# Performance work log

Measured on AMD Instinct MI355X. Metric: run time of the kernel, lower is better.

## Reference

```python
import jax, jax.numpy as jnp
import numpy as np
from jax import lax

FH, FW, STRIDE = 100, 160, 16
IMG_H, IMG_W = FH * STRIDE, FW * STRIDE
A = 9
PRE_NMS, POST_NMS = 6000, 300  # prediction-path caps (training=0)
IOU_THR = 0.7
NEG = jnp.float32(-1e9)


def _make_anchor_map():
    # classic 3 scales x 3 aspect ratios, stride-16 grid, (y1,x1,y2,x2)
    scales = np.array([128.0, 256.0, 512.0], np.float32)
    ratios = np.array([0.5, 1.0, 2.0], np.float32)
    hs = (scales[:, None] * np.sqrt(ratios)[None, :]).reshape(-1)  # [9]
    ws = (scales[:, None] / np.sqrt(ratios)[None, :]).reshape(-1)
    cy = ((np.arange(FH, dtype=np.float32) + 0.5) * STRIDE)[:, None, None]
    cx = ((np.arange(FW, dtype=np.float32) + 0.5) * STRIDE)[None, :, None]
    y1 = np.broadcast_to(cy - 0.5 * hs, (FH, FW, A))
    x1 = np.broadcast_to(cx - 0.5 * ws, (FH, FW, A))
    y2 = np.broadcast_to(cy + 0.5 * hs, (FH, FW, A))
    x2 = np.broadcast_to(cx + 0.5 * ws, (FH, FW, A))
    am = np.stack([y1, x1, y2, x2], axis=-1)  # [FH,FW,9,4]
    return jnp.asarray(am.reshape(1, FH, FW, A * 4))


def setup_inputs() -> dict:
    key = jax.random.key(0)
    ks = jax.random.split(key, 6)
    return {
        "input_image": jax.random.uniform(ks[0], (1, IMG_H, IMG_W, 3), jnp.float32),
        "feature_map": jax.random.normal(ks[1], (1, FH, FW, 512), jnp.float32),
        "anchor_map": _make_anchor_map(),
        "anchor_valid_map": jnp.ones((1, FH, FW, A), jnp.float32),
        "W1": 0.01 * jax.random.normal(ks[2], (3, 3, 512, 512), jnp.float32),
        "b1": jnp.zeros((512,), jnp.float32),
        "Wc": 0.01 * jax.random.normal(ks[3], (1, 1, 512, A), jnp.float32),
        "bc": jnp.zeros((A,), jnp.float32),
        "Wr": 0.01 * jax.random.normal(ks[4], (1, 1, 512, 4 * A), jnp.float32),
        "br": jnp.zeros((4 * A,), jnp.float32),
        "training": 0,
    }


def _conv(x, w, b):
    return lax.conv_general_dilated(
        x, w, (1, 1), "SAME", dimension_numbers=("NHWC", "HWIO", "NHWC")
    ) + b


def _iou_one_vs_all(box, boxes):
    yy1 = jnp.maximum(box[0], boxes[:, 0])
    xx1 = jnp.maximum(box[1], boxes[:, 1])
    yy2 = jnp.minimum(box[2], boxes[:, 2])
    xx2 = jnp.minimum(box[3], boxes[:, 3])
    inter = jnp.maximum(yy2 - yy1, 0.0) * jnp.maximum(xx2 - xx1, 0.0)
    a1 = jnp.maximum(box[2] - box[0], 0.0) * jnp.maximum(box[3] - box[1], 0.0)
    a2 = jnp.maximum(boxes[:, 2] - boxes[:, 0], 0.0) * jnp.maximum(boxes[:, 3] - boxes[:, 1], 0.0)
    return inter / (a1 + a2 - inter + 1e-8)


def _nms(boxes, scores, max_out, iou_thr):
    # greedy NMS with fixed iteration count (padded with zero boxes)
    def step(s, _):
        i = jnp.argmax(s)
        best = s[i]
        box = boxes[i]
        valid = best > NEG * 0.5
        ious = _iou_one_vs_all(box, boxes)
        s = jnp.where(ious > iou_thr, NEG, s)
        s = s.at[i].set(NEG)
        out = jnp.where(valid, box, jnp.zeros_like(box))
        return s, out

    _, sel = lax.scan(step, scores, None, length=max_out)
    return sel  # [max_out, 4]


def reference(input_image, feature_map, anchor_map, anchor_valid_map,
              W1, b1, Wc, bc, Wr, br, training):
    pre_nms = 12000 if training else PRE_NMS
    post_nms = 2000 if training else POST_NMS
    # RPN head convs
    y = jax.nn.relu(_conv(feature_map, W1, b1))
    scores_map = jax.nn.sigmoid(_conv(y, Wc, bc))          # [1,FH,FW,9]
    reg_map = _conv(y, Wr, br)                              # [1,FH,FW,36]
    # flatten (extract_valid)
    anchors = anchor_map.reshape(-1, 4)                     # [N,4] (y1,x1,y2,x2)
    obj = scores_map.reshape(-1)                            # [N]
    deltas = reg_map.reshape(-1, 4)                         # [N,4] (ty,tx,th,tw)
    # delta -> bbox decode (means=0, stds=1)
    ah = anchors[:, 2] - anchors[:, 0]
    aw = anchors[:, 3] - anchors[:, 1]
    acy = anchors[:, 0] + 0.5 * ah
    acx = anchors[:, 1] + 0.5 * aw
    cy = acy + deltas[:, 0] * ah
    cx = acx + deltas[:, 1] * aw
    h = ah * jnp.exp(deltas[:, 2])
    w = aw * jnp.exp(deltas[:, 3])
    props = jnp.stack([cy - 0.5 * h, cx - 0.5 * w, cy + 0.5 * h, cx + 0.5 * w], axis=1)
    # sort desc by score, keep top pre_nms
    sc, idx = lax.top_k(obj, pre_nms)
    props = props[idx]
    # clip to image
    img_h = jnp.float32(input_image.shape[1])
    img_w = jnp.float32(input_image.shape[2])
    tl = jnp.maximum(props[:, 0:2], 0.0)
    y2 = jnp.minimum(props[:, 2], img_h)[:, None]
    x2 = jnp.minimum(props[:, 3], img_w)[:, None]
    props = jnp.concatenate([tl, y2, x2], axis=1)
    # min-size filter (>=16 on each side), via score masking (jit-safe)
    hh = props[:, 2] - props[:, 0]
    ww = props[:, 3] - props[:, 1]
    sc = jnp.where((hh >= 16.0) & (ww >= 16.0), sc, NEG)
    proposals = _nms(props, sc, post_nms, IOU_THR)          # [post_nms,4], zero-padded
    return scores_map, reg_map, proposals
```

## Files before the change

kernel.cpp:

```cpp
#include <hip/hip_runtime.h>
#include <math.h>

#define FHh 100
#define FWw 160
#define CIN 512
#define COUT 512
#define NPIX 16000
#define NANCH 144000
#define PRE_NMS 6000
#define POST_NMS 300
#define EQCAP 8192

typedef double d4 __attribute__((ext_vector_type(4)));

__device__ __forceinline__ unsigned fkey(float x){
  unsigned b = __float_as_uint(x);
  return (b & 0x80000000u) ? ~b : (b | 0x80000000u);
}
__device__ __forceinline__ unsigned long long dkey(double x){
  unsigned long long u = (unsigned long long)__double_as_longlong(x);
  return (u & 0x8000000000000000ull) ? ~u : (u | 0x8000000000000000ull);
}
__device__ __forceinline__ unsigned long long shfl_u64(unsigned long long x, int lane){
  unsigned lo = (unsigned)x, hi = (unsigned)(x >> 32);
  lo = __shfl(lo, lane, 64);
  hi = __shfl(hi, lane, 64);
  return ((unsigned long long)hi << 32) | lo;
}

__global__ __launch_bounds__(256) void prep_all(
    const float* __restrict__ Wc, const float* __restrict__ Wr,
    double* __restrict__ WcT, double* __restrict__ WrT)
{
  const int gid = blockIdx.x*256 + threadIdx.x;
  const int n = gid >> 9, ci = gid & 511;
  if (n < 9) WcT[(size_t)n*512 + ci] = (double)Wc[ci*9 + n];
  else       WrT[(size_t)(n-9)*512 + ci] = (double)Wr[ci*36 + (n-9)];
}

__global__ __launch_bounds__(256, 2) void conv_gemm(
    const float* __restrict__ fm, const float* __restrict__ W1,
    const float* __restrict__ b1, double* __restrict__ yd)
{
  __shared__ double Ns[16*204];

  const int bid  = blockIdx.x;
  const int cg   = bid / 125;
  const int tile = bid - cg*125;
  const int rp   = tile / 5;
  const int xseg = tile - rp*5;
  const int x0   = xseg*32;
  const int row0 = rp*4;
  const int co0  = cg*128;

  const int tid  = threadIdx.x;
  const int lane = tid & 63;
  const int kl   = lane >> 4;
  const int cl   = lane & 15;
  const int wv   = tid >> 6;
  const int wr   = wv >> 1;
  const int wc   = wv & 1;

  double pf[4][4];

  auto APF_LOAD = [&](int kc){
    #pragma unroll
    for (int it = 0; it < 4; ++it){
      const int t  = it*256 + tid;
      const int px = t >> 2, kq = t & 3;
      const int nr = px / 34, nc = px - nr*34;
      const int row = row0 + nr - 1, col = x0 + nc - 1;
      const bool ok = (t < 816) && (row >= 0) && (row < FHh) && (col >= 0) && (col < FWw);
      if (ok){
        const float4 v = *(const float4*)(fm + ((size_t)(row*FWw + col))*CIN + kc*16 + kq*4);
        pf[it][0] = (double)v.x; pf[it][1] = (double)v.y;
        pf[it][2] = (double)v.z; pf[it][3] = (double)v.w;
      } else {
        pf[it][0] = pf[it][1] = pf[it][2] = pf[it][3] = 0.0;
      }
    }
  };
  auto APF_WRITE = [&](){
    #pragma unroll
    for (int it = 0; it < 4; ++it){
      const int t  = it*256 + tid;
      const int px = t >> 2, kq = t & 3;
      if (t < 816){
        #pragma unroll
        for (int u = 0; u < 4; ++u)
          Ns[(kq*4 + u)*204 + px] = pf[it][u];
      }
    }
  };

  d4 acc[4][4];
  #pragma unroll
  for (int mt = 0; mt < 4; ++mt)
    #pragma unroll
    for (int nt = 0; nt < 4; ++nt) acc[mt][nt] = (d4){0.0, 0.0, 0.0, 0.0};

  APF_LOAD(0);
  APF_WRITE();
  __syncthreads();

  const int abase_t = kl*204 + cl;
  const float* Bbase = W1 + (size_t)kl*512 + co0 + wc*64 + cl;

  #pragma unroll 1
  for (int kc = 0; kc < 32; ++kc){
    #pragma unroll 1
    for (int tap = 0; tap < 9; ++tap){
      if (tap == 7 && kc < 31) APF_LOAD(kc + 1);
      const float* Bt = Bbase + ((size_t)(tap*512 + kc*16))*512;
      double breg[16];
      #pragma unroll
      for (int k4 = 0; k4 < 4; ++k4)
        #pragma unroll
        for (int nt = 0; nt < 4; ++nt)
          breg[k4*4 + nt] = (double)Bt[k4*2048 + nt*16];
      const int ty = tap / 3;
      const int dy = ty - 1, dx = (tap - ty*3) - 1;
      const double* An = Ns + abase_t + (wr*2 + dy + 1)*34 + (dx + 1);
      __builtin_amdgcn_s_setprio(1);
      #pragma unroll
      for (int k4 = 0; k4 < 4; ++k4){
        const double a0 = An[k4*4*204 + 0*34 + 0];
        const double a1 = An[k4*4*204 + 0*34 + 16];
        const double a2 = An[k4*4*204 + 1*34 + 0];
        const double a3 = An[k4*4*204 + 1*34 + 16];
        const double b0 = breg[k4*4 + 0];
        const double b1v= breg[k4*4 + 1];
        const double b2 = breg[k4*4 + 2];
        const double b3 = breg[k4*4 + 3];
        acc[0][0] = __builtin_amdgcn_mfma_f64_16x16x4f64(a0, b0,  acc[0][0], 0, 0, 0);
        acc[0][1] = __builtin_amdgcn_mfma_f64_16x16x4f64(a0, b1v, acc[0][1], 0, 0, 0);
        acc[0][2] = __builtin_amdgcn_mfma_f64_16x16x4f64(a0, b2,  acc[0][2], 0, 0, 0);
        acc[0][3] = __builtin_amdgcn_mfma_f64_16x16x4f64(a0, b3,  acc[0][3], 0, 0, 0);
        acc[1][0] = __builtin_amdgcn_mfma_f64_16x16x4f64(a1, b0,  acc[1][0], 0, 0, 0);
        acc[1][1] = __builtin_amdgcn_mfma_f64_16x16x4f64(a1, b1v, acc[1][1], 0, 0, 0);
        acc[1][2] = __builtin_amdgcn_mfma_f64_16x16x4f64(a1, b2,  acc[1][2], 0, 0, 0);
        acc[1][3] = __builtin_amdgcn_mfma_f64_16x16x4f64(a1, b3,  acc[1][3], 0, 0, 0);
        acc[2][0] = __builtin_amdgcn_mfma_f64_16x16x4f64(a2, b0,  acc[2][0], 0, 0, 0);
        acc[2][1] = __builtin_amdgcn_mfma_f64_16x16x4f64(a2, b1v, acc[2][1], 0, 0, 0);
        acc[2][2] = __builtin_amdgcn_mfma_f64_16x16x4f64(a2, b2,  acc[2][2], 0, 0, 0);
        acc[2][3] = __builtin_amdgcn_mfma_f64_16x16x4f64(a2, b3,  acc[2][3], 0, 0, 0);
        acc[3][0] = __builtin_amdgcn_mfma_f64_16x16x4f64(a3, b0,  acc[3][0], 0, 0, 0);
        acc[3][1] = __builtin_amdgcn_mfma_f64_16x16x4f64(a3, b1v, acc[3][1], 0, 0, 0);
        acc[3][2] = __builtin_amdgcn_mfma_f64_16x16x4f64(a3, b2,  acc[3][2], 0, 0, 0);
        acc[3][3] = __builtin_amdgcn_mfma_f64_16x16x4f64(a3, b3,  acc[3][3], 0, 0, 0);
      }
      __builtin_amdgcn_s_setprio(0);
    }
    __syncthreads();
    if (kc < 31){
      APF_WRITE();
      __syncthreads();
    }
  }
  double bb[4];
  #pragma unroll
  for (int nt = 0; nt < 4; ++nt) bb[nt] = (double)b1[co0 + wc*64 + nt*16 + cl];
  #pragma unroll
  for (int mt = 0; mt < 4; ++mt){
    #pragma unroll
    for (int i = 0; i < 4; ++i){
      const int pxl = wr*64 + mt*16 + 4*i + kl;
      const int gpx = (row0 + (pxl >> 5))*FWw + x0 + (pxl & 31);
      double* yrow = yd + (size_t)gpx*CIN + co0 + wc*64 + cl;
      #pragma unroll
      for (int nt = 0; nt < 4; ++nt){
        yrow[nt*16] = fmax(acc[mt][nt][i] + bb[nt], 0.0);
      }
    }
  }
}

__global__ __launch_bounds__(256) void head2(
    const double* __restrict__ yd, const double* __restrict__ WcT, const float* __restrict__ bc,
    const double* __restrict__ WrT, const float* __restrict__ br,
    float* __restrict__ out, double* __restrict__ scored, double* __restrict__ regd)
{
  __shared__ double yl[8192];
  const int bid = blockIdx.x, t = threadIdx.x;
  const double2* src = (const double2*)(yd + (size_t)bid * 8192);
  double2* dst = (double2*)yl;
  for (int j = t; j < 4096; j += 256) dst[j] = src[j];
  __syncthreads();
  if (t < 180){
    const int n  = t % 45;
    const int pq = t / 45;
    const double* w = (n < 9) ? (WcT + (size_t)n*512) : (WrT + (size_t)(n-9)*512);
    const double* y0 = yl + (pq*4+0)*512;
    const double* y1 = yl + (pq*4+1)*512;
    const double* y2 = yl + (pq*4+2)*512;
    const double* y3 = yl + (pq*4+3)*512;
    double s0=0.0, s1=0.0, s2=0.0, s3=0.0;
    for (int ci = 0; ci < 512; ++ci){
      const double wv = w[ci];
      s0 = fma(y0[ci], wv, s0);
      s1 = fma(y1[ci], wv, s1);
      s2 = fma(y2[ci], wv, s2);
      s3 = fma(y3[ci], wv, s3);
    }
    const double sv[4] = {s0, s1, s2, s3};
    if (n < 9){
      const double bb = (double)bc[n];
      #pragma unroll
      for (int u = 0; u < 4; ++u){
        const double s = sv[u] + bb;
        const double sig = 1.0 / (1.0 + exp(-s));
        const int gi = (bid*16 + pq*4 + u)*9 + n;
        out[gi] = (float)sig;
        scored[gi] = sig;
      }
    } else {
      const int m = n - 9;
      const double bb = (double)br[m];
      #pragma unroll
      for (int u = 0; u < 4; ++u){
        const double s = sv[u] + bb;
        const int gi = (bid*16 + pq*4 + u)*36 + m;
        out[144000 + gi] = (float)s;
        regd[gi] = s;
      }
    }
  }
}

__global__ __launch_bounds__(256) void decode_hist(
    const float* __restrict__ amap, const double* __restrict__ scored,
    const double* __restrict__ regd, double* __restrict__ boxesd,
    unsigned* __restrict__ key32, unsigned long long* __restrict__ nmskey,
    unsigned* __restrict__ hist)
{
  const int i = blockIdx.x*256 + threadIdx.x;
  if (i >= NANCH) return;
  const double a0=(double)amap[4*i+0], a1=(double)amap[4*i+1];
  const double a2=(double)amap[4*i+2], a3=(double)amap[4*i+3];
  const double d0=regd[4*i+0], d1=regd[4*i+1], d2=regd[4*i+2], d3=regd[4*i+3];
  const double ah = a2 - a0, aw = a3 - a1;
  const double cy = a0 + 0.5*ah + d0*ah;
  const double cx = a1 + 0.5*aw + d1*aw;
  const double h = ah * exp(d2), w = aw * exp(d3);
  double y1 = cy - 0.5*h, x1 = cx - 0.5*w, y2 = cy + 0.5*h, x2 = cx + 0.5*w;
  y1 = fmax(y1, 0.0); x1 = fmax(x1, 0.0);
  y2 = fmin(y2, 1600.0); x2 = fmin(x2, 2560.0);
  boxesd[4*i+0]=y1; boxesd[4*i+1]=x1; boxesd[4*i+2]=y2; boxesd[4*i+3]=x2;
  const double obj = scored[i];
  const bool ok = (y2 - y1 >= 16.0) && (x2 - x1 >= 16.0);
  const unsigned k32 = fkey((float)obj);
  key32[i] = k32;
  nmskey[i] = ok ? dkey(obj) : dkey(-1e9);
  atomicAdd(&hist[k32 >> 16], 1u);
}

__global__ __launch_bounds__(1024) void scan_hi(const unsigned* __restrict__ hist, int* __restrict__ meta){
  __shared__ unsigned part[1024];
  const int t = threadIdx.x;
  unsigned s = 0;
  for (int j = 0; j < 64; ++j) s += hist[65535 - (t*64 + j)];
  part[t] = s;
  __syncthreads();
  for (int off = 1; off < 1024; off <<= 1){
    unsigned v = (t >= off) ? part[t - off] : 0u;
    __syncthreads();
    part[t] += v;
    __syncthreads();
  }
  const unsigned incl = part[t], excl = incl - s;
  if (excl < PRE_NMS && incl >= PRE_NMS){
    unsigned cum = excl;
    for (int j = 0; j < 64; ++j){
      const int bin = 65535 - (t*64 + j);
      const unsigned c = hist[bin];
      if (cum + c >= PRE_NMS){ meta[0] = bin; meta[1] = (int)cum; break; }
      cum += c;
    }
  }
}

__global__ __launch_bounds__(256) void hist_lo(const unsigned* __restrict__ key,
                                               const int* __restrict__ meta, unsigned* __restrict__ hist){
  const int i = blockIdx.x*256 + threadIdx.x;
  if (i < NANCH){
    const unsigned k = key[i];
    if ((int)(k >> 16) == meta[0]) atomicAdd(&hist[k & 0xFFFFu], 1u);
  }
}

__global__ __launch_bounds__(1024) void scan_lo(const unsigned* __restrict__ hist, int* __restrict__ meta){
  __shared__ unsigned part[1024];
  const int t = threadIdx.x;
  const unsigned G0 = (unsigned)meta[1];
  unsigned s = 0;
  for (int j = 0; j < 64; ++j) s += hist[65535 - (t*64 + j)];
  part[t] = s;
  __syncthreads();
  for (int off = 1; off < 1024; off <<= 1){
    unsigned v = (t >= off) ? part[t - off] : 0u;
    __syncthreads();
    part[t] += v;
    __syncthreads();
  }
  const unsigned incl = G0 + part[t], excl = incl - s;
  if (excl < PRE_NMS && incl >= PRE_NMS){
    unsigned cum = excl;
    for (int j = 0; j < 64; ++j){
      const int bin = 65535 - (t*64 + j);
      const unsigned c = hist[bin];
      if (cum + c >= PRE_NMS){
        meta[2] = (int)(((unsigned)meta[0] << 16) | (unsigned)bin);
        meta[3] = (int)cum;
        meta[4] = PRE_NMS - (int)cum;
        break;
      }
      cum += c;
    }
  }
}

__global__ __launch_bounds__(256) void compact_k(
    const unsigned* __restrict__ key, const unsigned long long* __restrict__ nmskey,
    const double* __restrict__ boxesd, const int* __restrict__ meta,
    int* __restrict__ cnt, double* __restrict__ selboxd,
    unsigned long long* __restrict__ selkey, int* __restrict__ eqidx)
{
  const int i = blockIdx.x*256 + threadIdx.x;
  if (i >= NANCH) return;
  const unsigned k = key[i];
  const unsigned T = (unsigned)meta[2];
  if (k > T){
    const int s = atomicAdd(&cnt[0], 1);
    selboxd[4*s+0]=boxesd[4*i+0]; selboxd[4*s+1]=boxesd[4*i+1];
    selboxd[4*s+2]=boxesd[4*i+2]; selboxd[4*s+3]=boxesd[4*i+3];
    selkey[s] = nmskey[i];
  } else if (k == T){
    const int e = atomicAdd(&cnt[1], 1);
    if (e < EQCAP) eqidx[e] = i;
  }
}

__global__ __launch_bounds__(256) void rankeq(
    const double* __restrict__ scored, const double* __restrict__ boxesd,
    const unsigned long long* __restrict__ nmskey,
    const int* __restrict__ meta, const int* __restrict__ cnt,
    const int* __restrict__ eqidx, double* __restrict__ selboxd,
    unsigned long long* __restrict__ selkey)
{
  __shared__ int eq[EQCAP];
  const int t = threadIdx.x;
  int E = cnt[1]; if (E > EQCAP) E = EQCAP;
  const int R = meta[4], G2 = meta[3];
  for (int j = t; j < E; j += 256) eq[j] = eqidx[j];
  __syncthreads();
  for (int j = t; j < E; j += 256){
    const int my = eq[j];
    const double smy = scored[my];
    int rank = 0;
    for (int k2 = 0; k2 < E; ++k2){
      const int ok = eq[k2];
      const double sk = scored[ok];
      rank += ((sk > smy) || (sk == smy && ok < my)) ? 1 : 0;
    }
    if (rank < R){
      const int s = G2 + rank;
      selboxd[4*s+0]=boxesd[4*my+0]; selboxd[4*s+1]=boxesd[4*my+1];
      selboxd[4*s+2]=boxesd[4*my+2]; selboxd[4*s+3]=boxesd[4*my+3];
      selkey[s] = nmskey[my];
    }
  }
}

__global__ __launch_bounds__(256) void rank_scatter(
    const unsigned long long* __restrict__ selkey, const double* __restrict__ selboxd,
    unsigned long long* __restrict__ skeys, double* __restrict__ sboxd)
{
  __shared__ unsigned long long k[PRE_NMS];
  const int t = threadIdx.x;
  for (int j = t; j < PRE_NMS; j += 256) k[j] = selkey[j];
  __syncthreads();
  const int j = blockIdx.x*256 + t;
  if (j >= PRE_NMS) return;
  const unsigned long long kj = k[j];
  int r = 0;
  for (int i = 0; i < PRE_NMS; i += 4){
    r += (int)((k[i+0] > kj) || (k[i+0] == kj && (i+0) < j));
    r += (int)((k[i+1] > kj) || (k[i+1] == kj && (i+1) < j));
    r += (int)((k[i+2] > kj) || (k[i+2] == kj && (i+2) < j));
    r += (int)((k[i+3] > kj) || (k[i+3] == kj && (i+3) < j));
  }
  skeys[r] = kj;
  sboxd[(size_t)r*4+0] = selboxd[(size_t)j*4+0];
  sboxd[(size_t)r*4+1] = selboxd[(size_t)j*4+1];
  sboxd[(size_t)r*4+2] = selboxd[(size_t)j*4+2];
  sboxd[(size_t)r*4+3] = selboxd[(size_t)j*4+3];
}

__global__ __launch_bounds__(256) void iou_bitmap(
    const double* __restrict__ sboxd, unsigned long long* __restrict__ rowbits)
{
  __shared__ double cbx[4096];
  const int g = blockIdx.y;
  const int r0 = blockIdx.x * 16;
  const int t = threadIdx.x;
  const int cbase = g * 1024;
  for (int e = t; e < 4096; e += 256){
    const int bi = cbase + (e >> 2);
    cbx[e] = (bi < PRE_NMS) ? sboxd[(size_t)bi*4 + (e & 3)] : 0.0;
  }
  __syncthreads();
  const int r = r0 + (t >> 4);
  const int w = t & 15;
  const double by1 = sboxd[(size_t)r*4+0], bx1 = sboxd[(size_t)r*4+1];
  const double by2 = sboxd[(size_t)r*4+2], bx2 = sboxd[(size_t)r*4+3];
  const double a1 = fmax(by2-by1, 0.0) * fmax(bx2-bx1, 0.0);
  unsigned long long bits = 0ull;
  for (int b = 0; b < 64; ++b){
    const int bcol = (b + w) & 63;
    const int j = cbase + w*64 + bcol;
    if (j < PRE_NMS){
      const int ce = (w*64 + bcol)*4;
      const double c0 = cbx[ce+0], c1 = cbx[ce+1], c2 = cbx[ce+2], c3 = cbx[ce+3];
      const double yy1 = fmax(by1, c0), xx1 = fmax(bx1, c1);
      const double yy2 = fmin(by2, c2), xx2 = fmin(bx2, c3);
      const double inter = fmax(yy2-yy1, 0.0) * fmax(xx2-xx1, 0.0);
      const double a2 = fmax(c2-c0, 0.0) * fmax(c3-c1, 0.0);
      const double iou = inter / (a1 + a2 - inter + 1e-8);
      if (iou > 0.7) bits |= (1ull << bcol);
    }
  }
  rowbits[(size_t)r*128 + g*16 + w] = bits;
}

__global__ __launch_bounds__(64) void greedy(
    const unsigned long long* __restrict__ skeys, const double* __restrict__ sboxd,
    const unsigned long long* __restrict__ rowbits, float* __restrict__ outp)
{
  const int t = threadIdx.x;
  const unsigned long long KEYTH = dkey(-5.0e8);
  int bad = PRE_NMS;
  for (int j = t; j < PRE_NMS; j += 64){
    if (skeys[j] <= KEYTH){ bad = j; break; }
  }
  #pragma unroll
  for (int off = 32; off > 0; off >>= 1){
    const int o = __shfl_down(bad, off, 64);
    bad = (o < bad) ? o : bad;
  }
  const int ilim = __builtin_amdgcn_readfirstlane(bad);

  auto maskfrom = [](int start) -> unsigned long long {
    if (start <= 0) return ~0ull;
    if (start >= 64) return 0ull;
    return (~0ull) << start;
  };
  unsigned long long s0 = maskfrom(ilim - t*64);
  unsigned long long s1 = (t < 30) ? maskfrom(ilim - (64 + t)*64) : ~0ull;

  int emitted = 0;
  for (int w = 0; w < 94 && emitted < POST_NMS; ++w){
    const unsigned long long sw = (w < 64) ? shfl_u64(s0, w) : shfl_u64(s1, w - 64);
    unsigned long long avail = ~sw;
    while (avail && emitted < POST_NMS){
      const int b = __ffsll((long long)avail) - 1;
      const int i = w*64 + b;
      if (t < 4) outp[4*emitted + t] = (float)sboxd[(size_t)i*4 + t];
      const unsigned long long r0 = rowbits[(size_t)i*128 + t];
      const unsigned long long r1 = (t < 30) ? rowbits[(size_t)i*128 + 64 + t] : 0ull;
      s0 |= r0; s1 |= r1;
      ++emitted;
      const unsigned long long rw = (w < 64) ? shfl_u64(r0, w) : shfl_u64(r1, w - 64);
      avail &= ~rw;
      avail &= ~(1ull << b);
    }
  }
  for (int r = emitted; r < POST_NMS; ++r)
    if (t < 4) outp[4*r + t] = 0.f;
}

extern "C" void kernel_launch(void* const* d_in, const int* in_sizes, int n_in,
                              void* d_out, int out_size, void* d_ws, size_t ws_size,
                              hipStream_t stream)
{
  const float* fm   = (const float*)d_in[1];
  const float* amap = (const float*)d_in[2];
  const float* W1   = (const float*)d_in[4];
  const float* b1   = (const float*)d_in[5];
  const float* Wc   = (const float*)d_in[6];
  const float* bc   = (const float*)d_in[7];
  const float* Wr   = (const float*)d_in[8];
  const float* br   = (const float*)d_in[9];
  float* out = (float*)d_out;

  char* base = (char*)d_ws;
  size_t off = 0;
  auto A = [&](size_t n) -> char* {
    char* p = base + off;
    off = (off + n + 255) & ~(size_t)255;
    return p;
  };
  double* yd      = (double*)A(65536000);
  double* WcT     = (double*)A(36864);
  double* WrT     = (double*)A(147456);
  double* scored  = (double*)A(1152000);
  double* regd    = (double*)A(4608000);
  unsigned* histc = (unsigned*)A(524328);
  double* boxesd              = (double*)A(4608000);
  unsigned long long* nmskey  = (unsigned long long*)A(1152000);
  unsigned* key32             = (unsigned*)A(576000);
  double* selboxd             = (double*)A(192000);
  unsigned long long* selkey  = (unsigned long long*)A(48000);
  unsigned long long* skeys   = (unsigned long long*)A(48000);
  double* sboxd               = (double*)A(192000);
  unsigned long long* rowbits = (unsigned long long*)A(6144000);
  int* eqidx                  = (int*)A(32768);

  unsigned* hist1 = histc;
  unsigned* hist2 = histc + 65536;
  int* cnt        = (int*)(histc + 131072);
  int* meta       = cnt + 2;

  hipMemsetAsync(histc, 0, (size_t)524328, stream);

  hipLaunchKernelGGL(prep_all, dim3(90), dim3(256), 0, stream,
                     Wc, Wr, WcT, WrT);
  hipLaunchKernelGGL(conv_gemm, dim3(500), dim3(256), 0, stream, fm, W1, b1, yd);
  hipLaunchKernelGGL(head2, dim3(1000), dim3(256), 0, stream, yd, WcT, bc, WrT, br, out, scored, regd);
  hipLaunchKernelGGL(decode_hist, dim3((NANCH + 255)/256), dim3(256), 0, stream,
                     amap, scored, regd, boxesd, key32, nmskey, hist1);
  hipLaunchKernelGGL(scan_hi, dim3(1), dim3(1024), 0, stream, hist1, meta);
  hipLaunchKernelGGL(hist_lo, dim3((NANCH + 255)/256), dim3(256), 0, stream, key32, meta, hist2);
  hipLaunchKernelGGL(scan_lo, dim3(1), dim3(1024), 0, stream, hist2, meta);
  hipLaunchKernelGGL(compact_k, dim3((NANCH + 255)/256), dim3(256), 0, stream,
                     key32, nmskey, boxesd, meta, cnt, selboxd, selkey, eqidx);
  hipLaunchKernelGGL(rankeq, dim3(1), dim3(256), 0, stream,
                     scored, boxesd, nmskey, meta, cnt, eqidx, selboxd, selkey);
  hipLaunchKernelGGL(rank_scatter, dim3((PRE_NMS + 255)/256), dim3(256), 0, stream,
                     selkey, selboxd, skeys, sboxd);
  hipLaunchKernelGGL(iou_bitmap, dim3(375, 6), dim3(256), 0, stream, sboxd, rowbits);
  hipLaunchKernelGGL(greedy, dim3(1), dim3(64), 0, stream, skeys, sboxd, rowbits, out + 720000);
}
```

Before: 2.003 ms.

## Compute RPN 1x1 head with FP64 MFMA using a padded transposed weight matrix

```diff
diff --git a/kernel.cpp b/kernel.cpp
--- a/kernel.cpp
+++ b/kernel.cpp
@@ -30,12 +30,14 @@
 
 __global__ __launch_bounds__(256) void prep_all(
     const float* __restrict__ Wc, const float* __restrict__ Wr,
-    double* __restrict__ WcT, double* __restrict__ WrT)
+    double* __restrict__ WT)
 {
   const int gid = blockIdx.x*256 + threadIdx.x;
-  const int n = gid >> 9, ci = gid & 511;
-  if (n < 9) WcT[(size_t)n*512 + ci] = (double)Wc[ci*9 + n];
-  else       WrT[(size_t)(n-9)*512 + ci] = (double)Wr[ci*36 + (n-9)];
+  const int k = gid / 48, n = gid - k*48;
+  double v = 0.0;
+  if (n < 9)       v = (double)Wc[k*9 + n];
+  else if (n < 45) v = (double)Wr[k*36 + (n-9)];
+  WT[gid] = v;
 }
 
 __global__ __launch_bounds__(256, 2) void conv_gemm(
@@ -175,53 +177,65 @@
   }
 }
 
-__global__ __launch_bounds__(256) void head2(
-    const double* __restrict__ yd, const double* __restrict__ WcT, const float* __restrict__ bc,
-    const double* __restrict__ WrT, const float* __restrict__ br,
+__global__ __launch_bounds__(64) void head2(
+    const double* __restrict__ yd, const double* __restrict__ WT,
+    const float* __restrict__ bc, const float* __restrict__ br,
     float* __restrict__ out, double* __restrict__ scored, double* __restrict__ regd)
 {
-  __shared__ double yl[8192];
-  const int bid = blockIdx.x, t = threadIdx.x;
-  const double2* src = (const double2*)(yd + (size_t)bid * 8192);
-  double2* dst = (double2*)yl;
-  for (int j = t; j < 4096; j += 256) dst[j] = src[j];
-  __syncthreads();
-  if (t < 180){
-    const int n  = t % 45;
-    const int pq = t / 45;
-    const double* w = (n < 9) ? (WcT + (size_t)n*512) : (WrT + (size_t)(n-9)*512);
-    const double* y0 = yl + (pq*4+0)*512;
-    const double* y1 = yl + (pq*4+1)*512;
-    const double* y2 = yl + (pq*4+2)*512;
-    const double* y3 = yl + (pq*4+3)*512;
-    double s0=0.0, s1=0.0, s2=0.0, s3=0.0;
-    for (int ci = 0; ci < 512; ++ci){
-      const double wv = w[ci];
-      s0 = fma(y0[ci], wv, s0);
-      s1 = fma(y1[ci], wv, s1);
-      s2 = fma(y2[ci], wv, s2);
-      s3 = fma(y3[ci], wv, s3);
-    }
-    const double sv[4] = {s0, s1, s2, s3};
-    if (n < 9){
-      const double bb = (double)bc[n];
-      #pragma unroll
-      for (int u = 0; u < 4; ++u){
-        const double s = sv[u] + bb;
+  __shared__ double yl[16*130];
+  const int bid = blockIdx.x;
+  const int t   = threadIdx.x;
+  const int kl  = t >> 4;
+  const int cl  = t & 15;
+
+  d4 acc[3];
+  acc[0] = (d4){0.0,0.0,0.0,0.0};
+  acc[1] = (d4){0.0,0.0,0.0,0.0};
+  acc[2] = (d4){0.0,0.0,0.0,0.0};
+
+  const double2* src = (const double2*)(yd + (size_t)bid*8192);
+
+  #pragma unroll 1
+  for (int c = 0; c < 4; ++c){
+    #pragma unroll
+    for (int j = 0; j < 16; ++j){
+      const double2 v = src[(size_t)j*256 + c*64 + t];
+      *(double2*)&yl[j*130 + t*2] = v;
+    }
+    __syncthreads();
+    const double* arow = yl + cl*130 + kl;
+    const double* brow = WT + ((size_t)c*128 + kl)*48 + cl;
+    #pragma unroll 8
+    for (int k4 = 0; k4 < 32; ++k4){
+      const double a  = arow[4*k4];
+      const double b0 = brow[(size_t)4*k4*48 + 0];
+      const double b1 = brow[(size_t)4*k4*48 + 16];
+      const double b2 = brow[(size_t)4*k4*48 + 32];
+      acc[0] = __builtin_amdgcn_mfma_f64_16x16x4f64(a, b0, acc[0], 0, 0, 0);
+      acc[1] = __builtin_amdgcn_mfma_f64_16x16x4f64(a, b1, acc[1], 0, 0, 0);
+      acc[2] = __builtin_amdgcn_mfma_f64_16x16x4f64(a, b2, acc[2], 0, 0, 0);
+    }
+    __syncthreads();
+  }
+
+  const int pxb = bid*16;
+  #pragma unroll
+  for (int nb = 0; nb < 3; ++nb){
+    const int n = nb*16 + cl;
+    #pragma unroll
+    for (int i = 0; i < 4; ++i){
+      const int gpx = pxb + 4*i + kl;
+      const double s0 = acc[nb][i];
+      if (n < 9){
+        const double s = s0 + (double)bc[n];
         const double sig = 1.0 / (1.0 + exp(-s));
-        const int gi = (bid*16 + pq*4 + u)*9 + n;
-        out[gi] = (float)sig;
-        scored[gi] = sig;
-      }
-    } else {
-      const int m = n - 9;
-      const double bb = (double)br[m];
-      #pragma unroll
-      for (int u = 0; u < 4; ++u){
-        const double s = sv[u] + bb;
-        const int gi = (bid*16 + pq*4 + u)*36 + m;
-        out[144000 + gi] = (float)s;
-        regd[gi] = s;
+        out[gpx*9 + n] = (float)sig;
+        scored[gpx*9 + n] = sig;
+      } else if (n < 45){
+        const int m = n - 9;
+        const double s = s0 + (double)br[m];
+        out[144000 + gpx*36 + m] = (float)s;
+        regd[gpx*36 + m] = s;
       }
     }
   }
@@ -500,8 +514,7 @@
     return p;
   };
   double* yd      = (double*)A(65536000);
-  double* WcT     = (double*)A(36864);
-  double* WrT     = (double*)A(147456);
+  double* WT      = (double*)A(196608);
   double* scored  = (double*)A(1152000);
   double* regd    = (double*)A(4608000);
   unsigned* histc = (unsigned*)A(524328);
@@ -522,10 +535,9 @@
 
   hipMemsetAsync(histc, 0, (size_t)524328, stream);
 
-  hipLaunchKernelGGL(prep_all, dim3(90), dim3(256), 0, stream,
-                     Wc, Wr, WcT, WrT);
+  hipLaunchKernelGGL(prep_all, dim3(96), dim3(256), 0, stream, Wc, Wr, WT);
   hipLaunchKernelGGL(conv_gemm, dim3(500), dim3(256), 0, stream, fm, W1, b1, yd);
-  hipLaunchKernelGGL(head2, dim3(1000), dim3(256), 0, stream, yd, WcT, bc, WrT, br, out, scored, regd);
+  hipLaunchKernelGGL(head2, dim3(1000), dim3(64), 0, stream, yd, WT, bc, br, out, scored, regd);
   hipLaunchKernelGGL(decode_hist, dim3((NANCH + 255)/256), dim3(256), 0, stream,
                      amap, scored, regd, boxesd, key32, nmskey, hist1);
   hipLaunchKernelGGL(scan_hi, dim3(1), dim3(1024), 0, stream, hist1, meta);
```

Measured after the change: 1.940 ms. -3.2%, faster.
